# Kernel tuning notes

Measured on AMD Instinct MI355X. Metric: run time of the kernel, lower is better.

The kernel has to match this reference:

```python
import jax, jax.numpy as jnp
import numpy as np

N_HEADS = 8
TOPK = 32


def setup_inputs() -> dict:
    key = jax.random.key(0)
    ks = jax.random.split(key, 6)
    N, L, Hd = 2, 2048, 512
    s = 1.0 / np.sqrt(Hd).astype(np.float32)
    return {
        "queries": jax.random.normal(ks[0], (N, L, Hd), jnp.float32),
        "keys": jax.random.normal(ks[1], (N, L, Hd), jnp.float32),
        "values": jax.random.normal(ks[2], (N, L, Hd), jnp.float32),
        "Wq": jax.random.normal(ks[3], (Hd, Hd), jnp.float32) * s,
        "bq": jnp.zeros((Hd,), jnp.float32),
        "Wk": jax.random.normal(ks[4], (Hd, Hd), jnp.float32) * s,
        "bk": jnp.zeros((Hd,), jnp.float32),
        "Wv": jax.random.normal(ks[5], (Hd, Hd), jnp.float32) * s,
        "bv": jnp.zeros((Hd,), jnp.float32),
    }


def reference(queries, keys, values, Wq, bq, Wk, bk, Wv, bv):
    N, L, Hd = queries.shape
    S = keys.shape[1]
    H = N_HEADS
    E = Hd // H
    q = (queries @ Wq.T + bq).reshape(N, L, H, E)
    k = (keys @ Wk.T + bk).reshape(N, S, H, E)
    v = (values @ Wv.T + bv).reshape(N, S, H, E)
    temp = 1.0 / np.sqrt(E).astype(np.float32)
    QK = jnp.einsum("nlhe,nshe->nhls", q, k)  # [N,H,L,S]
    topk = min(TOPK, S)
    _, idx = jax.lax.top_k(QK, topk)  # idx: [N,H,L,topk]
    ni = jnp.arange(N)[:, None, None, None]
    hi = jnp.arange(H)[None, :, None, None]
    li = jnp.arange(L)[None, None, :, None]
    keep = jnp.zeros(QK.shape, bool).at[ni, hi, li, idx].set(True)
    # torch: softmax(temp * (QK + mask)) with mask 0 on top-k, -inf elsewhere
    scores = jnp.where(keep, temp * QK, -jnp.inf)
    A = jax.nn.softmax(scores, axis=-1)  # dropout is identity in eval mode
    V = jnp.einsum("nhls,nshd->nlhd", A, v).reshape(N, L, Hd)
    return V, A
```

## Files before the change

### kernel.cpp

```cpp
#include <hip/hip_runtime.h>
#include <cstdint>
#include <cstddef>
#include <math.h>

#define NH     8
#define EH     64
#define HD     512
#define NBATCH 2
#define LSEQ   2048
#define TK     32


using f32x4  = __attribute__((ext_vector_type(4))) float;
using bf16x8 = __attribute__((ext_vector_type(8))) short;
using u16x8  = __attribute__((ext_vector_type(8))) unsigned short;

__device__ __forceinline__ unsigned short f2b(float f) {
    unsigned u = __float_as_uint(f);
    return (unsigned short)((u + 0x7FFFu + ((u >> 16) & 1u)) >> 16);
}
__device__ __forceinline__ unsigned f2key(float f) {
    unsigned u = __float_as_uint(f);
    return (u & 0x80000000u) ? ~u : (u | 0x80000000u);
}
__device__ __forceinline__ float key2f(unsigned k) {
    return __uint_as_float((k & 0x80000000u) ? (k ^ 0x80000000u) : ~k);
}
__device__ __forceinline__ unsigned umax2(unsigned a, unsigned b) { return a > b ? a : b; }

__global__ __launch_bounds__(256) void proj_kernel(
    const float* __restrict__ Xq, const float* __restrict__ Xk, const float* __restrict__ Xv,
    const float* __restrict__ Wq, const float* __restrict__ Bq,
    const float* __restrict__ Wk, const float* __restrict__ Bk,
    const float* __restrict__ Wv, const float* __restrict__ Bv,
    float* __restrict__ ws)
{
    const int z = blockIdx.z;
    const float* X = (z == 0) ? Xq : (z == 1) ? Xk : Xv;
    const float* W = (z == 0) ? Wq : (z == 1) ? Wk : Wv;
    const float* B = (z == 0) ? Bq : (z == 1) ? Bk : Bv;
    float* out = ws + (size_t)z * 2097152;
    unsigned short* khi = (unsigned short*)(ws + 6291456);

    __shared__ float4 Xs[64 * 8];
    __shared__ float4 Ws[64 * 8];
    __shared__ unsigned short kst[64 * 72];

    const int tid = threadIdx.x;
    const int tx = tid & 15, ty = tid >> 4;
    const int m0 = blockIdx.x * 64, n0 = blockIdx.y * 64;

    float acc[4][4];
    #pragma unroll
    for (int i = 0; i < 4; ++i)
        #pragma unroll
        for (int j = 0; j < 4; ++j) acc[i][j] = 0.f;

    for (int k0 = 0; k0 < HD; k0 += 32) {
        #pragma unroll
        for (int it = 0; it < 2; ++it) {
            int f = tid + it * 256;
            int row = f >> 3, c = f & 7;
            int cs = c ^ ((row >> 2) & 7);
            Xs[row * 8 + cs] = *(const float4*)&X[(size_t)(m0 + row) * HD + k0 + c * 4];
            Ws[row * 8 + cs] = *(const float4*)&W[(size_t)(n0 + row) * HD + k0 + c * 4];
        }
        __syncthreads();
        #pragma unroll
        for (int c = 0; c < 8; ++c) {
            float4 av[4], bv4[4];
            #pragma unroll
            for (int i = 0; i < 4; ++i) { int r = ty * 4 + i; av[i]  = Xs[r * 8 + (c ^ ((r >> 2) & 7))]; }
            #pragma unroll
            for (int j = 0; j < 4; ++j) { int r = tx * 4 + j; bv4[j] = Ws[r * 8 + (c ^ ((r >> 2) & 7))]; }
            #pragma unroll
            for (int i = 0; i < 4; ++i)
                #pragma unroll
                for (int j = 0; j < 4; ++j) {
                    acc[i][j] = fmaf(av[i].x, bv4[j].x, acc[i][j]);
                    acc[i][j] = fmaf(av[i].y, bv4[j].y, acc[i][j]);
                    acc[i][j] = fmaf(av[i].z, bv4[j].z, acc[i][j]);
                    acc[i][j] = fmaf(av[i].w, bv4[j].w, acc[i][j]);
                }
        }
        __syncthreads();
    }

    #pragma unroll
    for (int j = 0; j < 4; ++j) {
        int o = n0 + tx * 4 + j;
        float bb = B[o];
        int h = o >> 6, e = o & 63;
        #pragma unroll
        for (int i = 0; i < 4; ++i) {
            int m = m0 + ty * 4 + i;
            int n = m >> 11, s = m & 2047;
            float val = acc[i][j] + bb;
            int head = n * NH + h;
            out[(size_t)head * 131072 + (size_t)s * EH + e] = val;
            if (z == 1) kst[(ty * 4 + i) * 72 + e] = f2b(val);
        }
    }

    if (z == 1) {
        __syncthreads();
        const int head = (m0 >> 11) * NH + (n0 >> 6);
        const int kt0  = (m0 & 2047) >> 4;
        #pragma unroll
        for (int it = 0; it < 2; ++it) {
            int g = tid + it * 256;
            int lane_g = g & 63;
            int rest = g >> 6;
            int kt = rest >> 1, ksb = rest & 1;
            int s_loc = kt * 16 + (lane_g & 15);
            int e0 = ksb * 32 + ((lane_g >> 4) << 3);
            u16x8 vv = *(const u16x8*)&kst[s_loc * 72 + e0];
            size_t idx = ((((size_t)head * 128 + (kt0 + kt)) * 2 + ksb) * 64 + lane_g) * 8;
            *(u16x8*)&khi[idx] = vv;
        }
    }
}

__device__ __forceinline__ unsigned long long sort64_desc(unsigned long long v, int lane) {
    #pragma unroll
    for (int k = 2; k <= 64; k <<= 1)
        #pragma unroll
        for (int j = k >> 1; j >= 1; j >>= 1) {
            unsigned long long o = __shfl_xor(v, j, 64);
            bool up = ((lane & k) != 0);
            bool keepmin = (((lane & j) == 0) == up);
            unsigned long long lo = v < o ? v : o;
            unsigned long long hi = v > o ? v : o;
            v = keepmin ? lo : hi;
        }
    return v;
}
__device__ __forceinline__ unsigned long long merge_top64(unsigned long long a, unsigned long long b, int lane) {
    unsigned long long br = __shfl(b, 63 - lane, 64);
    unsigned long long m = a > br ? a : br;
    #pragma unroll
    for (int j = 32; j >= 1; j >>= 1) {
        unsigned long long o = __shfl_xor(m, j, 64);
        bool keepmax = ((lane & j) == 0);
        unsigned long long mx = m > o ? m : o;
        unsigned long long mn = m < o ? m : o;
        m = keepmax ? mx : mn;
    }
    return m;
}

__global__ __launch_bounds__(512, 4) void attn_kernel(
    const float* __restrict__ ws, float* __restrict__ outV, float* __restrict__ outA)
{
    const float* qw = ws;
    const float* kw = ws + 2097152;
    const float* vw = ws + 4194304;
    const unsigned short* khi = (const unsigned short*)(ws + 6291456);

    __shared__ unsigned short scores16[16 * 2048];
    __shared__ float qs[EH * 16];
    __shared__ unsigned short candArr[8 * 256];

    const int tid  = threadIdx.x;
    const int lane = tid & 63;
    const int uwv  = __builtin_amdgcn_readfirstlane(tid) >> 6;

    unsigned bid = blockIdx.x;
    unsigned id  = (bid & 7u) * 256u + (bid >> 3);
    const int head = (int)(id >> 7);
    const int l0   = (int)(id & 127u) * 16;
    const size_t headoff = (size_t)head * 131072;

    #pragma unroll
    for (int it = 0; it < 2; ++it) {
        int i = tid + it * 512;
        int row = i & 15, e = i >> 4;
        qs[i] = qw[headoff + (size_t)(l0 + row) * EH + e];
    }
    __syncthreads();

    {
        bf16x8 afrag[2];
        #pragma unroll
        for (int ks = 0; ks < 2; ++ks)
            #pragma unroll
            for (int j = 0; j < 8; ++j) {
                int e = ks * 32 + ((lane >> 4) << 3) + j;
                afrag[ks][j] = (short)f2b(qs[e * 16 + (lane & 15)]);
            }

        #pragma unroll
        for (int kt = 0; kt < 16; ++kt) {
            f32x4 acc = (f32x4)(0.f);
            int ktg = uwv * 16 + kt;
            #pragma unroll
            for (int ks = 0; ks < 2; ++ks) {
                bf16x8 b = *(const bf16x8*)(khi + (size_t)head * 131072 +
                              ((((size_t)ktg * 2 + ks) * 64 + lane) << 3));
                acc = __builtin_amdgcn_mfma_f32_16x16x32_bf16(afrag[ks], b, acc, 0, 0, 0);
            }
            int key = uwv * 256 + kt * 16 + (lane & 15);
            int rbase = (lane >> 4) << 2;
            #pragma unroll
            for (int reg = 0; reg < 4; ++reg)
                scores16[(rbase + reg) * 2048 + key] = (unsigned short)(f2key(acc[reg]) >> 16);
        }
    }
    __syncthreads();

    unsigned short* cand = candArr + uwv * 256;
    const unsigned long long lmlt = (1ull << lane) - 1ull;
    int selS[2]; float selW[2];

    #pragma unroll
    for (int rr2 = 0; rr2 < 2; ++rr2) {
        const int r = 2 * uwv + rr2;
        const int lrow = l0 + r;
        const unsigned* srow32 = (const unsigned*)(scores16 + r * 2048);

        unsigned pk[16];
        #pragma unroll
        for (int t = 0; t < 16; ++t) pk[t] = srow32[t * 64 + lane];

        unsigned mx = 0;
        #pragma unroll
        for (int t = 0; t < 16; ++t) {
            unsigned a = pk[t] & 0xFFFFu, b = pk[t] >> 16;
            mx = umax2(mx, umax2(a, b));
        }
        {
            unsigned v = mx;
            #pragma unroll
            for (int k = 2; k <= 64; k <<= 1)
                #pragma unroll
                for (int j = k >> 1; j >= 1; j >>= 1) {
                    unsigned o = __shfl_xor(v, j);
                    bool up = ((lane & k) == 0);
                    bool keepmin = (((lane & j) == 0) == up);
                    unsigned lo = v < o ? v : o, hi = v > o ? v : o;
                    v = keepmin ? lo : hi;
                }
            mx = __shfl(v, 32);
        }
        const unsigned tau16 = mx;
        const float tauf = key2f(tau16 << 16);
        const unsigned thr16 = f2key(tauf - 0.35f) >> 16;

        int Nc = 0;
        #pragma unroll
        for (int t = 0; t < 16; ++t) {
            unsigned vv = pk[t];
            unsigned i0 = (unsigned)((t * 64 + lane) * 2);
            bool c0 = (vv & 0xFFFFu) >= thr16;
            bool c1 = (vv >> 16) >= thr16;
            unsigned long long b0 = __ballot(c0);
            if (c0) {
                int p = Nc + __popcll(b0 & lmlt);
                if (p < 256) cand[p] = (unsigned short)i0;
            }
            Nc += __popcll(b0);
            unsigned long long b1 = __ballot(c1);
            if (c1) {
                int p = Nc + __popcll(b1 & lmlt);
                if (p < 256) cand[p] = (unsigned short)(i0 + 1);
            }
            Nc += __popcll(b1);
        }
        if (Nc > 256) Nc = 256;
        const int nch = (Nc + 63) >> 6;

        const float* qrow = qw + headoff + (size_t)lrow * EH;
        float4 qv[16];
        #pragma unroll
        for (int c4 = 0; c4 < 16; ++c4) qv[c4] = *(const float4*)&qrow[c4 * 4];

        unsigned long long best = 0ull;
        for (int c = 0; c < nch; ++c) {
            int p = c * 64 + lane;
            bool valid = p < Nc;
            int si = valid ? (int)cand[p] : 0;
            const float* krow = kw + headoff + (size_t)si * EH;
            float sc = 0.f;
            #pragma unroll
            for (int c4 = 0; c4 < 16; ++c4) {
                float4 kv = *(const float4*)&krow[c4 * 4];
                sc = fmaf(qv[c4].x, kv.x, sc);
                sc = fmaf(qv[c4].y, kv.y, sc);
                sc = fmaf(qv[c4].z, kv.z, sc);
                sc = fmaf(qv[c4].w, kv.w, sc);
            }
            unsigned long long comp = valid
                ? ((((unsigned long long)f2key(sc)) << 32) | (unsigned)(~si))
                : 0ull;
            comp = sort64_desc(comp, lane);
            best = (c == 0) ? comp : merge_top64(best, comp, lane);
        }

        unsigned key32 = (unsigned)(best >> 32);
        int si = (int)(~((unsigned)best)) & 2047;
        float sc = key2f(key32);
        float M = __shfl(sc, 0);
        float ee = (lane < TK) ? __expf(0.125f * (sc - M)) : 0.f;
        float Z = ee;
        #pragma unroll
        for (int d = 1; d < 64; d <<= 1) Z += __shfl_xor(Z, d);
        selS[rr2] = si;
        selW[rr2] = ee / Z;
    }

    float* abuf = (float*)((char*)scores16 + uwv * 8192);
    #pragma unroll
    for (int rr2 = 0; rr2 < 2; ++rr2) {
        const int lrow = l0 + 2 * uwv + rr2;
        float4* ab4 = (float4*)abuf;
        const float4 z4 = make_float4(0.f, 0.f, 0.f, 0.f);
        #pragma unroll
        for (int u = 0; u < 8; ++u) ab4[u * 64 + lane] = z4;
        if (lane < TK) abuf[selS[rr2]] = selW[rr2];
        float* Arow = outA + ((size_t)head * 2048 + lrow) * 2048;
        #pragma unroll
        for (int u = 0; u < 8; ++u)
            *(float4*)&Arow[(u * 64 + lane) * 4] = ab4[u * 64 + lane];

        float acc = 0.f;
        int   siv = selS[rr2];
        unsigned wbits = __float_as_uint(selW[rr2]);
        #pragma unroll
        for (int i = 0; i < TK; ++i) {
            int s_i   = __builtin_amdgcn_readlane(siv, i);
            float w_i = __uint_as_float((unsigned)__builtin_amdgcn_readlane((int)wbits, i));
            acc = fmaf(w_i, vw[headoff + (size_t)s_i * EH + lane], acc);
        }
        const int n = head >> 3, h = head & 7;
        outV[((size_t)(n * 2048 + lrow)) * 512 + h * 64 + lane] = acc;
    }
}

extern "C" void kernel_launch(void* const* d_in, const int* in_sizes, int n_in,
                              void* d_out, int out_size, void* d_ws, size_t ws_size,
                              hipStream_t stream)
{
    (void)in_sizes; (void)n_in; (void)out_size; (void)ws_size;
    const float* q  = (const float*)d_in[0];
    const float* k  = (const float*)d_in[1];
    const float* v  = (const float*)d_in[2];
    const float* Wq = (const float*)d_in[3];
    const float* bq = (const float*)d_in[4];
    const float* Wk = (const float*)d_in[5];
    const float* bk = (const float*)d_in[6];
    const float* Wv = (const float*)d_in[7];
    const float* bv = (const float*)d_in[8];
    float* ws   = (float*)d_ws;
    float* outV = (float*)d_out;
    float* outA = outV + (size_t)NBATCH * LSEQ * HD;

    proj_kernel<<<dim3(64, 8, 3), 256, 0, stream>>>(q, k, v, Wq, bq, Wk, bk, Wv, bv, ws);
    attn_kernel<<<dim3(2048, 1, 1), 512, 0, stream>>>(ws, outV, outA);
}
```

Before: 221.6 us.

## Zero attention matrix inside projection kernel and transpose score tile layout

The zero-fill of the dense 2048x2048-per-head attention output moves into the projection GEMM's k-loop, where each thread issues a few float4 zero stores per iteration. The attention kernel then only scatters the 32 selected weights per row. The shared-memory score tile is stored key-major with an XOR swizzle so each wave loads both of its rows in one packed pass. This tries to hide the large output write behind compute-bound GEMM work, but it adds write traffic to the projection kernel and relies on kernel ordering on the stream.

Result: slower. 233.3 us (+5.2%).

```diff
diff --git a/kernel.cpp b/kernel.cpp
--- a/kernel.cpp
+++ b/kernel.cpp
@@ -14,6 +14,10 @@
 using f32x4  = __attribute__((ext_vector_type(4))) float;
 using bf16x8 = __attribute__((ext_vector_type(8))) short;
 using u16x8  = __attribute__((ext_vector_type(8))) unsigned short;
+using u16x4  = __attribute__((ext_vector_type(4))) unsigned short;
+
+#define A_TOTAL4 16777216ull
+#define PROJ_THREADS 393216ull
 
 __device__ __forceinline__ unsigned short f2b(float f) {
     unsigned u = __float_as_uint(f);
@@ -33,7 +37,7 @@
     const float* __restrict__ Wq, const float* __restrict__ Bq,
     const float* __restrict__ Wk, const float* __restrict__ Bk,
     const float* __restrict__ Wv, const float* __restrict__ Bv,
-    float* __restrict__ ws)
+    float* __restrict__ ws, float* __restrict__ outA)
 {
     const int z = blockIdx.z;
     const float* X = (z == 0) ? Xq : (z == 1) ? Xk : Xv;
@@ -49,6 +53,10 @@
     const int tid = threadIdx.x;
     const int tx = tid & 15, ty = tid >> 4;
     const int m0 = blockIdx.x * 64, n0 = blockIdx.y * 64;
+    const int lin = (blockIdx.z * gridDim.y + blockIdx.y) * gridDim.x + blockIdx.x;
+    const size_t gtid = (size_t)lin * 256 + tid;
+    float4* outA4 = (float4*)outA;
+    const float4 z4 = make_float4(0.f, 0.f, 0.f, 0.f);
 
     float acc[4][4];
     #pragma unroll
@@ -56,7 +64,8 @@
         #pragma unroll
         for (int j = 0; j < 4; ++j) acc[i][j] = 0.f;
 
-    for (int k0 = 0; k0 < HD; k0 += 32) {
+    int cc = 0;
+    for (int k0 = 0; k0 < HD; k0 += 32, ++cc) {
         #pragma unroll
         for (int it = 0; it < 2; ++it) {
             int f = tid + it * 256;
@@ -64,6 +73,11 @@
             int cs = c ^ ((row >> 2) & 7);
             Xs[row * 8 + cs] = *(const float4*)&X[(size_t)(m0 + row) * HD + k0 + c * 4];
             Ws[row * 8 + cs] = *(const float4*)&W[(size_t)(n0 + row) * HD + k0 + c * 4];
+        }
+        #pragma unroll
+        for (int j = 0; j < 3; ++j) {
+            size_t zi = gtid + (size_t)(cc * 3 + j) * PROJ_THREADS;
+            if (zi < A_TOTAL4) outA4[zi] = z4;
         }
         __syncthreads();
         #pragma unroll
@@ -157,7 +171,7 @@
     const float* vw = ws + 4194304;
     const unsigned short* khi = (const unsigned short*)(ws + 6291456);
 
-    __shared__ unsigned short scores16[16 * 2048];
+    __shared__ unsigned short scores16[2048 * 16];
     __shared__ float qs[EH * 16];
     __shared__ unsigned short candArr[8 * 256];
 
@@ -201,9 +215,12 @@
             }
             int key = uwv * 256 + kt * 16 + (lane & 15);
             int rbase = (lane >> 4) << 2;
+            int p = rbase ^ (key & 12);
+            u16x4 s4;
             #pragma unroll
             for (int reg = 0; reg < 4; ++reg)
-                scores16[(rbase + reg) * 2048 + key] = (unsigned short)(f2key(acc[reg]) >> 16);
+                s4[reg] = (unsigned short)(f2key(acc[reg]) >> 16);
+            *(u16x4*)&scores16[key * 16 + p] = s4;
         }
     }
     __syncthreads();
@@ -212,21 +229,24 @@
     const unsigned long long lmlt = (1ull << lane) - 1ull;
     int selS[2]; float selW[2];
 
+    const int r0 = 2 * uwv;
+    unsigned pk[32];
+    #pragma unroll
+    for (int t = 0; t < 32; ++t) {
+        int key = t * 64 + lane;
+        int p0 = r0 ^ (key & 12);
+        pk[t] = *(const unsigned*)&scores16[key * 16 + p0];
+    }
+
     #pragma unroll
     for (int rr2 = 0; rr2 < 2; ++rr2) {
-        const int r = 2 * uwv + rr2;
-        const int lrow = l0 + r;
-        const unsigned* srow32 = (const unsigned*)(scores16 + r * 2048);
-
-        unsigned pk[16];
-        #pragma unroll
-        for (int t = 0; t < 16; ++t) pk[t] = srow32[t * 64 + lane];
+        const int lrow = l0 + r0 + rr2;
 
         unsigned mx = 0;
         #pragma unroll
-        for (int t = 0; t < 16; ++t) {
-            unsigned a = pk[t] & 0xFFFFu, b = pk[t] >> 16;
-            mx = umax2(mx, umax2(a, b));
+        for (int t = 0; t < 32; ++t) {
+            unsigned a = rr2 ? (pk[t] >> 16) : (pk[t] & 0xFFFFu);
+            mx = umax2(mx, a);
         }
         {
             unsigned v = mx;
@@ -248,23 +268,15 @@
 
         int Nc = 0;
         #pragma unroll
-        for (int t = 0; t < 16; ++t) {
-            unsigned vv = pk[t];
-            unsigned i0 = (unsigned)((t * 64 + lane) * 2);
-            bool c0 = (vv & 0xFFFFu) >= thr16;
-            bool c1 = (vv >> 16) >= thr16;
-            unsigned long long b0 = __ballot(c0);
-            if (c0) {
-                int p = Nc + __popcll(b0 & lmlt);
-                if (p < 256) cand[p] = (unsigned short)i0;
+        for (int t = 0; t < 32; ++t) {
+            unsigned a = rr2 ? (pk[t] >> 16) : (pk[t] & 0xFFFFu);
+            bool c = a >= thr16;
+            unsigned long long b = __ballot(c);
+            if (c) {
+                int p = Nc + __popcll(b & lmlt);
+                if (p < 256) cand[p] = (unsigned short)(t * 64 + lane);
             }
-            Nc += __popcll(b0);
-            unsigned long long b1 = __ballot(c1);
-            if (c1) {
-                int p = Nc + __popcll(b1 & lmlt);
-                if (p < 256) cand[p] = (unsigned short)(i0 + 1);
-            }
-            Nc += __popcll(b1);
+            Nc += __popcll(b);
         }
         if (Nc > 256) Nc = 256;
         const int nch = (Nc + 63) >> 6;
@@ -308,19 +320,11 @@
         selW[rr2] = ee / Z;
     }
 
-    float* abuf = (float*)((char*)scores16 + uwv * 8192);
     #pragma unroll
     for (int rr2 = 0; rr2 < 2; ++rr2) {
-        const int lrow = l0 + 2 * uwv + rr2;
-        float4* ab4 = (float4*)abuf;
-        const float4 z4 = make_float4(0.f, 0.f, 0.f, 0.f);
-        #pragma unroll
-        for (int u = 0; u < 8; ++u) ab4[u * 64 + lane] = z4;
-        if (lane < TK) abuf[selS[rr2]] = selW[rr2];
+        const int lrow = l0 + r0 + rr2;
         float* Arow = outA + ((size_t)head * 2048 + lrow) * 2048;
-        #pragma unroll
-        for (int u = 0; u < 8; ++u)
-            *(float4*)&Arow[(u * 64 + lane) * 4] = ab4[u * 64 + lane];
+        if (lane < TK) Arow[selS[rr2]] = selW[rr2];
 
         float acc = 0.f;
         int   siv = selS[rr2];
@@ -354,6 +358,6 @@
     float* outV = (float*)d_out;
     float* outA = outV + (size_t)NBATCH * LSEQ * HD;
 
-    proj_kernel<<<dim3(64, 8, 3), 256, 0, stream>>>(q, k, v, Wq, bq, Wk, bk, Wv, bv, ws);
+    proj_kernel<<<dim3(64, 8, 3), 256, 0, stream>>>(q, k, v, Wq, bq, Wk, bk, Wv, bv, ws, outA);
     attn_kernel<<<dim3(2048, 1, 1), 512, 0, stream>>>(ws, outV, outA);
 }
```
